# Performance work log

Measured on AMD Instinct MI355X. Metric: run time of the kernel, lower is better.

## Reference

```python
import jax, jax.numpy as jnp
import numpy as np

B, H, DH = 1, 16, 128
HID, MLP = 2048, 8192
LT, LI = 256, 2048
L = LT + LI


def _layernorm(x, eps=1e-6):
    mu = jnp.mean(x, axis=-1, keepdims=True)
    var = jnp.mean((x - mu) ** 2, axis=-1, keepdims=True)
    return (x - mu) * jax.lax.rsqrt(var + eps)


def _rmsnorm(x, scale, eps=1e-6):
    rr = jax.lax.rsqrt(jnp.mean(x * x, axis=-1, keepdims=True) + eps)
    return x * rr * scale


def _apply_rope(x, pe):
    # x: (B,H,L,D) -> (B,H,L,D/2,1,2); pe: (B,1,L,D/2,2,2)
    xs = x.reshape(*x.shape[:-1], -1, 1, 2)
    out = pe[..., 0] * xs[..., 0] + pe[..., 1] * xs[..., 1]  # (B,H,L,D/2,2)
    return out.reshape(x.shape)


def _qkv_split(x, w, b):
    Bv, Lv, _ = x.shape
    qkv = (x @ w + b).reshape(Bv, Lv, 3, H, DH).transpose(2, 0, 3, 1, 4)  # K B H L D
    return qkv[0], qkv[1], qkv[2]


def setup_inputs() -> dict:
    key = jax.random.key(0)
    ks = jax.random.split(key, 16)
    s = 0.02
    inp = {
        'img': jax.random.normal(ks[0], (B, LI, HID), jnp.float32),
        'txt': jax.random.normal(ks[1], (B, LT, HID), jnp.float32),
        'vec': jax.random.normal(ks[2], (B, HID), jnp.float32),
        'img_mod_w': s * jax.random.normal(ks[3], (HID, 6 * HID), jnp.float32),
        'img_mod_b': jnp.zeros((6 * HID,), jnp.float32),
        'txt_mod_w': s * jax.random.normal(ks[4], (HID, 6 * HID), jnp.float32),
        'txt_mod_b': jnp.zeros((6 * HID,), jnp.float32),
        'img_qkv_w': s * jax.random.normal(ks[5], (HID, 3 * HID), jnp.float32),
        'img_qkv_b': jnp.zeros((3 * HID,), jnp.float32),
        'img_q_scale': jnp.ones((DH,), jnp.float32),
        'img_k_scale': jnp.ones((DH,), jnp.float32),
        'txt_qkv_w': s * jax.random.normal(ks[6], (HID, 3 * HID), jnp.float32),
        'txt_qkv_b': jnp.zeros((3 * HID,), jnp.float32),
        'txt_q_scale': jnp.ones((DH,), jnp.float32),
        'txt_k_scale': jnp.ones((DH,), jnp.float32),
        'img_proj_w': s * jax.random.normal(ks[7], (HID, HID), jnp.float32),
        'img_proj_b': jnp.zeros((HID,), jnp.float32),
        'txt_proj_w': s * jax.random.normal(ks[8], (HID, HID), jnp.float32),
        'txt_proj_b': jnp.zeros((HID,), jnp.float32),
        'img_mlp_w1': s * jax.random.normal(ks[9], (HID, MLP), jnp.float32),
        'img_mlp_b1': jnp.zeros((MLP,), jnp.float32),
        'img_mlp_w2': s * jax.random.normal(ks[10], (MLP, HID), jnp.float32),
        'img_mlp_b2': jnp.zeros((HID,), jnp.float32),
        'txt_mlp_w1': s * jax.random.normal(ks[11], (HID, MLP), jnp.float32),
        'txt_mlp_b1': jnp.zeros((MLP,), jnp.float32),
        'txt_mlp_w2': s * jax.random.normal(ks[12], (MLP, HID), jnp.float32),
        'txt_mlp_b2': jnp.zeros((HID,), jnp.float32),
    }
    # Real RoPE rotation matrices [[cos,-sin],[sin,cos]]: (1,1,L,DH/2,2,2)
    pos = jnp.arange(L, dtype=jnp.float32)
    freqs = 1.0 / (10000.0 ** (jnp.arange(DH // 2, dtype=jnp.float32) / (DH // 2)))
    ang = pos[:, None] * freqs[None, :]
    c, sn = jnp.cos(ang), jnp.sin(ang)
    pe = jnp.stack([jnp.stack([c, -sn], -1), jnp.stack([sn, c], -1)], -2)  # (L,DH/2,2,2)
    inp['pe'] = pe[None, None]
    return inp


def reference(img, txt, vec, pe,
              img_mod_w, img_mod_b, txt_mod_w, txt_mod_b,
              img_qkv_w, img_qkv_b, img_q_scale, img_k_scale,
              txt_qkv_w, txt_qkv_b, txt_q_scale, txt_k_scale,
              img_proj_w, img_proj_b, txt_proj_w, txt_proj_b,
              img_mlp_w1, img_mlp_b1, img_mlp_w2, img_mlp_b2,
              txt_mlp_w1, txt_mlp_b1, txt_mlp_w2, txt_mlp_b2):
    # AdaLN modulation: SiLU(vec) @ W -> 6 chunks of (B,1,HID)
    im = jnp.split(jax.nn.silu(vec) @ img_mod_w + img_mod_b, 6, axis=-1)
    i_sh1, i_sc1, i_g1, i_sh2, i_sc2, i_g2 = [m[:, None, :] for m in im]
    tm = jnp.split(jax.nn.silu(vec) @ txt_mod_w + txt_mod_b, 6, axis=-1)
    t_sh1, t_sc1, t_g1, t_sh2, t_sc2, t_g2 = [m[:, None, :] for m in tm]

    img_mod = (1 + i_sc1) * _layernorm(img) + i_sh1
    iq, ik, iv = _qkv_split(img_mod, img_qkv_w, img_qkv_b)
    iq = _rmsnorm(iq, img_q_scale)
    ik = _rmsnorm(ik, img_k_scale)

    txt_mod = (1 + t_sc1) * _layernorm(txt) + t_sh1
    tq, tk, tv = _qkv_split(txt_mod, txt_qkv_w, txt_qkv_b)
    tq = _rmsnorm(tq, txt_q_scale)
    tk = _rmsnorm(tk, txt_k_scale)

    # concat text then image along sequence (B,H,L,D)
    q = jnp.concatenate([tq, iq], axis=2)
    k = jnp.concatenate([tk, ik], axis=2)
    v = jnp.concatenate([tv, iv], axis=2)
    q = _apply_rope(q, pe)
    k = _apply_rope(k, pe)

    scores = jnp.einsum('bhqd,bhkd->bhqk', q, k) / np.float32(np.sqrt(DH))
    a = jax.nn.softmax(scores, axis=-1)
    o = jnp.einsum('bhqk,bhkd->bhqd', a, v)
    attn = o.transpose(0, 2, 1, 3).reshape(o.shape[0], -1, H * DH)  # (B,L,HID)

    txt_a, img_a = attn[:, :LT], attn[:, LT:]

    img = img + i_g1 * (img_a @ img_proj_w + img_proj_b)
    h = (1 + i_sc2) * _layernorm(img) + i_sh2
    h = jax.nn.gelu(h @ img_mlp_w1 + img_mlp_b1, approximate=True)
    img = img + i_g2 * (h @ img_mlp_w2 + img_mlp_b2)

    txt = txt + t_g1 * (txt_a @ txt_proj_w + txt_proj_b)
    h = (1 + t_sc2) * _layernorm(txt) + t_sh2
    h = jax.nn.gelu(h @ txt_mlp_w1 + txt_mlp_b1, approximate=True)
    txt = txt + t_g2 * (h @ txt_mlp_w2 + txt_mlp_b2)

    return img, txt
```

## Files before the change

### kernel.cpp

```cpp
#include <hip/hip_runtime.h>

using u16 = unsigned short;
typedef __bf16 bf16x8 __attribute__((ext_vector_type(8)));
typedef float f32x4 __attribute__((ext_vector_type(4)));

__device__ inline u16 f2bf(float f){
  unsigned u = __float_as_uint(f);
  u += 0x7fff + ((u >> 16) & 1);
  return (u16)(u >> 16);
}
__device__ inline float bf2f(u16 u){ return __uint_as_float((unsigned)u << 16); }

__device__ inline float wredsum(float v){
  #pragma unroll
  for (int o = 32; o; o >>= 1) v += __shfl_xor(v, o, 64);
  return v;
}
__device__ inline float wredmax(float v){
  #pragma unroll
  for (int o = 32; o; o >>= 1) v = fmaxf(v, __shfl_xor(v, o, 64));
  return v;
}

__device__ inline void gld16(const u16* g, u16* lds){
  __builtin_amdgcn_global_load_lds(
      (const __attribute__((address_space(1))) unsigned int*)g,
      (__attribute__((address_space(3))) unsigned int*)lds, 16, 0, 0);
}

__global__ void mod_matvec_k(const float* __restrict__ vec,
    const float* __restrict__ wi, const float* __restrict__ bi,
    const float* __restrict__ wt, const float* __restrict__ bt,
    float* __restrict__ oi, float* __restrict__ ot)
{
  __shared__ float sv[2048];
  __shared__ float red[4][64];
  int tid = threadIdx.x;
  for (int i = tid; i < 2048; i += 256){ float v = vec[i]; sv[i] = v / (1.0f + __expf(-v)); }
  __syncthreads();
  int j0 = blockIdx.x * 64;
  bool ist = j0 >= 12288;
  const float* w = ist ? wt : wi;
  const float* b = ist ? bt : bi;
  float* o = ist ? ot : oi;
  int col = (ist ? j0 - 12288 : j0) + (tid & 63);
  int kq = tid >> 6;
  float acc = 0.f;
  const float* wp = w + col;
  for (int k = kq * 512; k < kq * 512 + 512; ++k) acc += sv[k] * wp[(long long)k * 12288];
  red[kq][tid & 63] = acc;
  __syncthreads();
  if (kq == 0){
    o[col] = red[0][tid] + red[1][tid] + red[2][tid] + red[3][tid] + b[col];
  }
}

__global__ void tcast_k(const float* __restrict__ in, u16* __restrict__ out, int K, int N)
{
  __shared__ float tile[32][33];
  int n0 = blockIdx.x * 32, k0 = blockIdx.y * 32;
  int tid = threadIdx.x;
  int r = tid >> 3, c4 = (tid & 7) * 4;
  float4 v = *(const float4*)&in[(long long)(k0 + r) * N + n0 + c4];
  tile[r][c4 + 0] = v.x; tile[r][c4 + 1] = v.y; tile[r][c4 + 2] = v.z; tile[r][c4 + 3] = v.w;
  __syncthreads();
  int n = tid >> 3, kq = (tid & 7) * 4;
  ushort4 o;
  o.x = f2bf(tile[kq + 0][n]);
  o.y = f2bf(tile[kq + 1][n]);
  o.z = f2bf(tile[kq + 2][n]);
  o.w = f2bf(tile[kq + 3][n]);
  *(ushort4*)&out[(long long)(n0 + n) * K + k0 + kq] = o;
}

__global__ void ln_mod_k(const float* __restrict__ x,
    const float* __restrict__ sh, const float* __restrict__ sc,
    u16* __restrict__ out)
{
  int row = blockIdx.x, tid = threadIdx.x;
  const float* xr = x + (long long)row * 2048;
  float v[8]; float s = 0.f, s2 = 0.f;
  #pragma unroll
  for (int j = 0; j < 8; ++j){ v[j] = xr[tid + j * 256]; s += v[j]; s2 += v[j] * v[j]; }
  s = wredsum(s); s2 = wredsum(s2);
  __shared__ float red[4][2];
  int wave = tid >> 6, lane = tid & 63;
  if (lane == 0){ red[wave][0] = s; red[wave][1] = s2; }
  __syncthreads();
  float S1 = red[0][0] + red[1][0] + red[2][0] + red[3][0];
  float S2 = red[0][1] + red[1][1] + red[2][1] + red[3][1];
  float mu = S1 * (1.0f / 2048.0f);
  float var = S2 * (1.0f / 2048.0f) - mu * mu;
  float rs = rsqrtf(var + 1e-6f);
  u16* orow = out + (long long)row * 2048;
  #pragma unroll
  for (int j = 0; j < 8; ++j){
    int c = tid + j * 256;
    orow[c] = f2bf((1.0f + sc[c]) * (v[j] - mu) * rs + sh[c]);
  }
}

__global__ void qkv_post_k(const float* __restrict__ qkv, int pos0,
    const float* __restrict__ qs, const float* __restrict__ ks,
    const float* __restrict__ pe,
    u16* __restrict__ Q, u16* __restrict__ Ko, u16* __restrict__ Vt)
{
  __shared__ u16 vs[128][72];
  int h = blockIdx.y;
  int t0 = blockIdx.x * 64;
  int tid = threadIdx.x, wave = tid >> 6, lane = tid & 63;
  for (int it = 0; it < 16; ++it){
    int tl = it * 4 + wave;
    int t = t0 + tl;
    const float* rp = qkv + (long long)t * 6144 + h * 128;
    float q0 = rp[lane],        q1 = rp[lane + 64];
    float k0 = rp[2048 + lane], k1 = rp[2048 + lane + 64];
    float v0 = rp[4096 + lane], v1 = rp[4096 + lane + 64];
    float qss = wredsum(q0 * q0 + q1 * q1);
    float kss = wredsum(k0 * k0 + k1 * k1);
    float rq = rsqrtf(qss * (1.0f / 128.0f) + 1e-6f) * 0.08838834764831845f;
    float rk = rsqrtf(kss * (1.0f / 128.0f) + 1e-6f);
    float qn0 = q0 * rq * qs[lane], qn1 = q1 * rq * qs[lane + 64];
    float kn0 = k0 * rk * ks[lane], kn1 = k1 * rk * ks[lane + 64];
    int pos = pos0 + t;
    const float* peb = pe + (long long)pos * 256;
    bool odd = lane & 1;
    float4 p0 = *(const float4*)&peb[(lane >> 1) * 4];
    float4 p1 = *(const float4*)&peb[128 + (lane >> 1) * 4];
    float c00 = odd ? p0.z : p0.x, c01 = odd ? p0.w : p0.y;
    float c10 = odd ? p1.z : p1.x, c11 = odd ? p1.w : p1.y;
    float qp0 = __shfl_xor(qn0, 1, 64), qp1 = __shfl_xor(qn1, 1, 64);
    float kp0 = __shfl_xor(kn0, 1, 64), kp1 = __shfl_xor(kn1, 1, 64);
    float qe0 = odd ? qp0 : qn0, qo0 = odd ? qn0 : qp0;
    float qe1 = odd ? qp1 : qn1, qo1 = odd ? qn1 : qp1;
    float ke0 = odd ? kp0 : kn0, ko0 = odd ? kn0 : kp0;
    float ke1 = odd ? kp1 : kn1, ko1 = odd ? kn1 : kp1;
    u16* Qr = Q  + ((long long)h * 2304 + pos) * 128;
    u16* Kr = Ko + ((long long)h * 2304 + pos) * 128;
    Qr[lane]      = f2bf(c00 * qe0 + c01 * qo0);
    Qr[lane + 64] = f2bf(c10 * qe1 + c11 * qo1);
    Kr[lane]      = f2bf(c00 * ke0 + c01 * ko0);
    Kr[lane + 64] = f2bf(c10 * ke1 + c11 * ko1);
    vs[lane][tl]      = f2bf(v0);
    vs[lane + 64][tl] = f2bf(v1);
  }
  __syncthreads();
  int dd = tid >> 1, co = (tid & 1) * 32;
  u16* vr = Vt + ((long long)h * 128 + dd) * 2304 + pos0 + t0 + co;
  #pragma unroll
  for (int u = 0; u < 8; ++u)
    *(ushort4*)(vr + u * 4) = *(const ushort4*)&vs[dd][co + u * 4];
}

__global__ void softmax16_k(u16* __restrict__ S)
{
  long long base = (long long)blockIdx.y * 2304 * 2304 + (long long)blockIdx.x * 2304;
  u16* row = S + base;
  int tid = threadIdx.x;
  float v[9]; float m = -3.0e38f;
  #pragma unroll
  for (int j = 0; j < 9; ++j){ v[j] = bf2f(row[tid + j * 256]); m = fmaxf(m, v[j]); }
  m = wredmax(m);
  __shared__ float red[4];
  int wave = tid >> 6, lane = tid & 63;
  if (lane == 0) red[wave] = m;
  __syncthreads();
  m = fmaxf(fmaxf(red[0], red[1]), fmaxf(red[2], red[3]));
  float s = 0.f;
  #pragma unroll
  for (int j = 0; j < 9; ++j){ v[j] = __expf(v[j] - m); s += v[j]; }
  s = wredsum(s);
  __syncthreads();
  if (lane == 0) red[wave] = s;
  __syncthreads();
  s = red[0] + red[1] + red[2] + red[3];
  float r = 1.0f / s;
  #pragma unroll
  for (int j = 0; j < 9; ++j) row[tid + j * 256] = f2bf(v[j] * r);
}

template<int MODE>
__global__ __launch_bounds__(512)
void gemm8_k(const u16* __restrict__ Ai, const u16* __restrict__ At, int lda,
             const u16* __restrict__ Bi, const u16* __restrict__ Bt, int ldb,
             const float* __restrict__ bias_i, const float* __restrict__ bias_t,
             const float* __restrict__ res_i,  const float* __restrict__ res_t,
             const float* __restrict__ gate_i, const float* __restrict__ gate_t,
             void* __restrict__ Ci, void* __restrict__ Ct, int ldc, int K)
{
  constexpr int BK = 64;
  constexpr int MR = 4, NR = 2;
  constexpr int AI = 2, BI = 2;

  __shared__ u16 As[2][128 * BK];
  __shared__ u16 Bs[2][128 * BK];

  const int tid  = threadIdx.x;
  const int lane = tid & 63;
  const int wave = tid >> 6;
  const int wm = wave >> 2;
  const int wn = wave & 3;

  const int bx = blockIdx.x;
  const int by = blockIdx.y;
  const bool ist = bx >= 16;
  const int rb = ist ? bx - 16 : bx;
  const u16* Ab = (ist ? At : Ai) + (long long)rb * 128 * lda;
  const u16* Bb = (ist ? Bt : Bi) + (long long)by * 128 * ldb;
  const float* bias = ist ? bias_t : bias_i;
  const float* res  = ist ? res_t  : res_i;
  const float* gate = ist ? gate_t : gate_i;
  void* C = ist ? Ct : Ci;

  const int srow = wave * 8 + (lane >> 3);
  const int sgo  = ((lane & 7) ^ ((lane >> 3) & 7)) * 8;
  const u16* agp[AI]; const u16* bgp[BI];
  int alo[AI], blo[BI];
  #pragma unroll
  for (int i = 0; i < AI; ++i){
    agp[i] = Ab + (long long)(i * 64 + srow) * lda + sgo;
    alo[i] = (i * 64 + wave * 8) * BK;
  }
  #pragma unroll
  for (int i = 0; i < BI; ++i){
    bgp[i] = Bb + (long long)(i * 64 + srow) * ldb + sgo;
    blo[i] = (i * 64 + wave * 8) * BK;
  }

  const int arow0 = wm * 64;
  const int frow  = lane & 15;
  const int fx    = lane & 7;
  const int j0    = lane >> 4;

  f32x4 acc[MR][NR] = {};

  #pragma unroll
  for (int i = 0; i < AI; ++i) gld16(agp[i], &As[0][alo[i]]);
  #pragma unroll
  for (int i = 0; i < BI; ++i) gld16(bgp[i], &Bs[0][blo[i]]);
  __builtin_amdgcn_sched_barrier(0);

  const int nt = K / BK;
  for (int t = 0; t < nt; ++t){
    if (t + 1 < nt){
      int k0 = (t + 1) * BK;
      int nb = (t + 1) & 1;
      #pragma unroll
      for (int i = 0; i < AI; ++i) gld16(agp[i] + k0, &As[nb][alo[i]]);
      #pragma unroll
      for (int i = 0; i < BI; ++i) gld16(bgp[i] + k0, &Bs[nb][blo[i]]);
      __builtin_amdgcn_sched_barrier(0);
      asm volatile("s_waitcnt vmcnt(4)" ::: "memory");
    } else {
      asm volatile("s_waitcnt vmcnt(0)" ::: "memory");
    }
    __builtin_amdgcn_sched_barrier(0);
    __builtin_amdgcn_s_barrier();
    __builtin_amdgcn_sched_barrier(0);

    const u16* as = As[t & 1];
    const u16* bs = Bs[t & 1];
    #pragma unroll
    for (int s = 0; s < 2; ++s){
      const int oct = (s * 4 + j0) ^ fx;
      bf16x8 bfr[NR];
      #pragma unroll
      for (int nn = 0; nn < NR; ++nn)
        bfr[nn] = *(const bf16x8*)&bs[(wn * 32 + nn * 16 + frow) * BK + oct * 8];
      __builtin_amdgcn_s_setprio(1);
      #pragma unroll
      for (int m = 0; m < MR; ++m){
        bf16x8 af = *(const bf16x8*)&as[(arow0 + m * 16 + frow) * BK + oct * 8];
        #pragma unroll
        for (int nn = 0; nn < NR; ++nn)
          acc[m][nn] = __builtin_amdgcn_mfma_f32_16x16x32_bf16(af, bfr[nn], acc[m][nn], 0, 0, 0);
      }
      __builtin_amdgcn_s_setprio(0);
    }
    __builtin_amdgcn_sched_barrier(0);
    __builtin_amdgcn_s_barrier();
    __builtin_amdgcn_sched_barrier(0);
  }

  const int lr = (lane >> 4) * 4;
  const int lc = lane & 15;
  const long long rowb = (long long)rb * 128 + arow0;
  const long long colb = (long long)by * 128 + wn * 32;
  #pragma unroll
  for (int mi = 0; mi < MR; ++mi){
    #pragma unroll
    for (int ni = 0; ni < NR; ++ni){
      long long col = colb + ni * 16 + lc;
      float bv = bias ? bias[col] : 0.0f;
      #pragma unroll
      for (int j = 0; j < 4; ++j){
        long long row = rowb + mi * 16 + lr + j;
        float v = acc[mi][ni][j] + bv;
        long long ci = row * (long long)ldc + col;
        if constexpr (MODE == 0) ((float*)C)[ci] = v;
        else if constexpr (MODE == 2) ((float*)C)[ci] = res[ci] + gate[col] * v;
        else {
          float z2 = 1.5957691216057308f * (v + 0.044715f * v * v * v);
          ((u16*)C)[ci] = f2bf(v / (1.0f + __expf(-z2)));
        }
      }
    }
  }
}

template<int BM, int BN, int MODE>
__global__ __launch_bounds__(256)
void gemm_k(const u16* __restrict__ A, int lda, long long abstr,
            const u16* __restrict__ B, int ldb, long long bbstr,
            void* __restrict__ C, int ldc, long long cbstr,
            int K)
{
  constexpr int BK  = 32;
  constexpr int WGM = BM / 64;
  constexpr int WGN = 4 / WGM;
  constexpr int WTN = BN / WGN;
  constexpr int NFR = WTN / 16;
  constexpr int CA  = BM / 64;
  constexpr int CB  = BN / 64;

  __shared__ u16 As[2][BM * BK];
  __shared__ u16 Bs[2][BN * BK];
  const int tid  = threadIdx.x;
  const int lane = tid & 63;
  const int wave = tid >> 6;
  const int wr = (wave / WGN) * 64;
  const int wc = (wave % WGN) * WTN;

  const u16* Ab = A + (long long)blockIdx.z * abstr + (long long)blockIdx.x * BM * lda;
  const u16* Bb = B + (long long)blockIdx.z * bbstr + (long long)blockIdx.y * BN * ldb;

  const int srow = lane >> 2;
  const int scol = (lane & 3) * 8;
  const u16* agp[CA]; int aro[CA];
  const u16* bgp[CB]; int bro[CB];
  #pragma unroll
  for (int c = 0; c < CA; ++c){
    int r0 = (c * 4 + wave) * 16;
    agp[c] = Ab + (long long)(r0 + srow) * lda + scol;
    aro[c] = r0 * BK;
  }
  #pragma unroll
  for (int c = 0; c < CB; ++c){
    int r0 = (c * 4 + wave) * 16;
    bgp[c] = Bb + (long long)(r0 + srow) * ldb + scol;
    bro[c] = r0 * BK;
  }

  #pragma unroll
  for (int c = 0; c < CA; ++c) gld16(agp[c], &As[0][aro[c]]);
  #pragma unroll
  for (int c = 0; c < CB; ++c) gld16(bgp[c], &Bs[0][bro[c]]);
  __syncthreads();

  f32x4 acc[4][NFR] = {};
  const int nt = K / BK;
  int cur = 0;
  for (int t = 0; t < nt; ++t){
    int nxt = cur ^ 1;
    if (t + 1 < nt){
      int ko = (t + 1) * BK;
      #pragma unroll
      for (int c = 0; c < CA; ++c) gld16(agp[c] + ko, &As[nxt][aro[c]]);
      #pragma unroll
      for (int c = 0; c < CB; ++c) gld16(bgp[c] + ko, &Bs[nxt][bro[c]]);
    }
    bf16x8 af[4], bfr[NFR];
    #pragma unroll
    for (int i = 0; i < 4; ++i)
      af[i] = *(const bf16x8*)&As[cur][(wr + i * 16 + (lane & 15)) * BK + (lane >> 4) * 8];
    #pragma unroll
    for (int i = 0; i < NFR; ++i)
      bfr[i] = *(const bf16x8*)&Bs[cur][(wc + i * 16 + (lane & 15)) * BK + (lane >> 4) * 8];
    #pragma unroll
    for (int mi = 0; mi < 4; ++mi)
      #pragma unroll
      for (int ni = 0; ni < NFR; ++ni)
        acc[mi][ni] = __builtin_amdgcn_mfma_f32_16x16x32_bf16(af[mi], bfr[ni], acc[mi][ni], 0, 0, 0);
    __syncthreads();
    cur = nxt;
  }

  const int lr = (lane >> 4) * 4;
  const int lc = lane & 15;
  const long long rowb = (long long)blockIdx.x * BM + wr;
  const long long colb = (long long)blockIdx.y * BN + wc;
  const long long cb = (long long)blockIdx.z * cbstr;
  #pragma unroll
  for (int mi = 0; mi < 4; ++mi){
    #pragma unroll
    for (int ni = 0; ni < NFR; ++ni){
      long long col = colb + ni * 16 + lc;
      #pragma unroll
      for (int j = 0; j < 4; ++j){
        long long row = rowb + mi * 16 + lr + j;
        float v = acc[mi][ni][j];
        long long ci = cb + row * ldc + col;
        if constexpr (MODE == 0) ((float*)C)[ci] = v;
        else ((u16*)C)[ci] = f2bf(v);
      }
    }
  }
}

extern "C" void kernel_launch(void* const* d_in, const int* in_sizes, int n_in,
                              void* d_out, int out_size, void* d_ws, size_t ws_size,
                              hipStream_t stream)
{
  const float* img        = (const float*)d_in[0];
  const float* txt        = (const float*)d_in[1];
  const float* vec        = (const float*)d_in[2];
  const float* img_mod_w  = (const float*)d_in[3];
  const float* img_mod_b  = (const float*)d_in[4];
  const float* txt_mod_w  = (const float*)d_in[5];
  const float* txt_mod_b  = (const float*)d_in[6];
  const float* img_qkv_w  = (const float*)d_in[7];
  const float* img_qkv_b  = (const float*)d_in[8];
  const float* img_q_s    = (const float*)d_in[9];
  const float* img_k_s    = (const float*)d_in[10];
  const float* txt_qkv_w  = (const float*)d_in[11];
  const float* txt_qkv_b  = (const float*)d_in[12];
  const float* txt_q_s    = (const float*)d_in[13];
  const float* txt_k_s    = (const float*)d_in[14];
  const float* img_proj_w = (const float*)d_in[15];
  const float* img_proj_b = (const float*)d_in[16];
  const float* txt_proj_w = (const float*)d_in[17];
  const float* txt_proj_b = (const float*)d_in[18];
  const float* img_mlp_w1 = (const float*)d_in[19];
  const float* img_mlp_b1 = (const float*)d_in[20];
  const float* img_mlp_w2 = (const float*)d_in[21];
  const float* img_mlp_b2 = (const float*)d_in[22];
  const float* txt_mlp_w1 = (const float*)d_in[23];
  const float* txt_mlp_b1 = (const float*)d_in[24];
  const float* txt_mlp_w2 = (const float*)d_in[25];
  const float* txt_mlp_b2 = (const float*)d_in[26];
  const float* pe         = (const float*)d_in[27];

  char* ws = (char*)d_ws;
  size_t off = 0;
  auto alloc = [&](size_t b){ void* p = ws + off; off = (off + b + 255) & ~(size_t)255; return p; };

  u16* wq_i = (u16*)alloc(6144ll * 2048 * 2);
  u16* wq_t = (u16*)alloc(6144ll * 2048 * 2);
  u16* wp_i = (u16*)alloc(2048ll * 2048 * 2);
  u16* wp_t = (u16*)alloc(2048ll * 2048 * 2);
  u16* w1_i = (u16*)alloc(8192ll * 2048 * 2);
  u16* w1_t = (u16*)alloc(8192ll * 2048 * 2);
  u16* w2_i = (u16*)alloc(2048ll * 8192 * 2);
  u16* w2_t = (u16*)alloc(2048ll * 8192 * 2);
  float* mod_i = (float*)alloc(12288 * 4);
  float* mod_t = (float*)alloc(12288 * 4);
  u16* Qb   = (u16*)alloc(16ll * 2304 * 128 * 2);
  u16* Kb   = (u16*)alloc(16ll * 2304 * 128 * 2);
  u16* Vt   = (u16*)alloc(16ll * 2304 * 128 * 2);
  u16* attn = (u16*)alloc(2304ll * 2048 * 2);
  char* big = (char*)alloc(4ll * 2304 * 2304 * 4);

  size_t s16_bytes = 16ll * 2304 * 2304 * 2;
  size_t off_before_s16 = off;
  u16* S16 = (u16*)alloc(s16_bytes);
  const bool merged_attn = (off <= ws_size);
  if (!merged_attn) off = off_before_s16;

  u16*   xin_i = (u16*)big;
  u16*   xin_t = (u16*)(big + 8388608);
  float* qkv_i = (float*)(big + 9437184);
  float* qkv_t = (float*)(big + 59768832);
  u16*   S4   = (u16*)big;
  float* y1_i  = (float*)big;
  float* y1_t  = (float*)(big + 16777216);
  u16*   ln2_i = (u16*)(big + 18874368);
  u16*   ln2_t = (u16*)(big + 27262976);
  u16*   h_i   = (u16*)(big + 28311552);
  u16*   h_t   = (u16*)(big + 61865984);

  mod_matvec_k<<<384, 256, 0, stream>>>(vec, img_mod_w, img_mod_b, txt_mod_w, txt_mod_b, mod_i, mod_t);

  tcast_k<<<dim3(192, 64), 256, 0, stream>>>(img_qkv_w, wq_i, 2048, 6144);
  tcast_k<<<dim3(192, 64), 256, 0, stream>>>(txt_qkv_w, wq_t, 2048, 6144);
  tcast_k<<<dim3(64, 64),  256, 0, stream>>>(img_proj_w, wp_i, 2048, 2048);
  tcast_k<<<dim3(64, 64),  256, 0, stream>>>(txt_proj_w, wp_t, 2048, 2048);
  tcast_k<<<dim3(256, 64), 256, 0, stream>>>(img_mlp_w1, w1_i, 2048, 8192);
  tcast_k<<<dim3(256, 64), 256, 0, stream>>>(txt_mlp_w1, w1_t, 2048, 8192);
  tcast_k<<<dim3(64, 256), 256, 0, stream>>>(img_mlp_w2, w2_i, 8192, 2048);
  tcast_k<<<dim3(64, 256), 256, 0, stream>>>(txt_mlp_w2, w2_t, 8192, 2048);

  ln_mod_k<<<2048, 256, 0, stream>>>(img, mod_i, mod_i + 2048, xin_i);
  ln_mod_k<<<256,  256, 0, stream>>>(txt, mod_t, mod_t + 2048, xin_t);

  gemm8_k<0><<<dim3(18, 48), 512, 0, stream>>>(xin_i, xin_t, 2048, wq_i, wq_t, 2048,
      img_qkv_b, txt_qkv_b, nullptr, nullptr, nullptr, nullptr, qkv_i, qkv_t, 6144, 2048);

  qkv_post_k<<<dim3(32, 16), 256, 0, stream>>>(qkv_i, 256, img_q_s, img_k_s, pe, Qb, Kb, Vt);
  qkv_post_k<<<dim3(4, 16),  256, 0, stream>>>(qkv_t, 0,   txt_q_s, txt_k_s, pe, Qb, Kb, Vt);

  if (merged_attn){
    gemm_k<128,128,1><<<dim3(18, 18, 16), 256, 0, stream>>>(Qb, 128, 2304ll * 128, Kb, 128, 2304ll * 128,
        S16, 2304, 2304ll * 2304, 128);
    softmax16_k<<<dim3(2304, 16), 256, 0, stream>>>(S16);
    gemm_k<128,64,1><<<dim3(18, 2, 16), 256, 0, stream>>>(S16, 2304, 2304ll * 2304, Vt, 2304, 128ll * 2304,
        attn, 2048, 128, 2304);
  } else {
    for (int g = 0; g < 4; ++g){
      const u16* Qg = Qb + (long long)g * 4 * 2304 * 128;
      const u16* Kg = Kb + (long long)g * 4 * 2304 * 128;
      const u16* Vg = Vt + (long long)g * 4 * 128 * 2304;
      gemm_k<128,128,1><<<dim3(18, 18, 4), 256, 0, stream>>>(Qg, 128, 2304ll * 128, Kg, 128, 2304ll * 128,
          S4, 2304, 2304ll * 2304, 128);
      softmax16_k<<<dim3(2304, 4), 256, 0, stream>>>(S4);
      gemm_k<128,64,1><<<dim3(18, 2, 4), 256, 0, stream>>>(S4, 2304, 2304ll * 2304, Vg, 2304, 128ll * 2304,
          attn + g * 4 * 128, 2048, 128, 2304);
    }
  }

  gemm8_k<2><<<dim3(18, 16), 512, 0, stream>>>(attn + 256 * 2048, attn, 2048, wp_i, wp_t, 2048,
      img_proj_b, txt_proj_b, img, txt, mod_i + 4096, mod_t + 4096, y1_i, y1_t, 2048, 2048);

  ln_mod_k<<<2048, 256, 0, stream>>>(y1_i, mod_i + 6144, mod_i + 8192, ln2_i);
  ln_mod_k<<<256,  256, 0, stream>>>(y1_t, mod_t + 6144, mod_t + 8192, ln2_t);

  gemm8_k<3><<<dim3(18, 64), 512, 0, stream>>>(ln2_i, ln2_t, 2048, w1_i, w1_t, 2048,
      img_mlp_b1, txt_mlp_b1, nullptr, nullptr, nullptr, nullptr, h_i, h_t, 8192, 2048);

  float* out_img = (float*)d_out;
  float* out_txt = out_img + 2048ll * 2048;
  gemm8_k<2><<<dim3(18, 16), 512, 0, stream>>>(h_i, h_t, 8192, w2_i, w2_t, 8192,
      img_mlp_b2, txt_mlp_b2, y1_i, y1_t, mod_i + 10240, mod_t + 10240, out_img, out_txt, 2048, 8192);
}
```

Measured before the change: 906.3 us.

## Batch weight transpose-casts into one launch and remap GEMM workgroups across XCDs

Merges the eight separate weight transpose-and-cast launches into a single grid kernel that picks its matrix through a per-matrix block-offset table, which removes per-launch overhead and tail gaps between launches. It also remaps workgroup ids in gemm8_k so that consecutive tiles land on the same XCD (ids are strided by 8), with the aim of better L2 reuse of shared A and B tiles. The remap assumes the tile count is divisible by 8 and adds a short index search per block in the cast kernel.

```diff
diff --git a/kernel.cpp b/kernel.cpp
--- a/kernel.cpp
+++ b/kernel.cpp
@@ -55,10 +55,27 @@
   }
 }
 
-__global__ void tcast_k(const float* __restrict__ in, u16* __restrict__ out, int K, int N)
+struct TcArgs {
+  const float* in[8];
+  u16* out[8];
+  int K[8];
+  int N[8];
+  int base[9];
+};
+
+__global__ void tcast8_k(TcArgs a)
 {
   __shared__ float tile[32][33];
-  int n0 = blockIdx.x * 32, k0 = blockIdx.y * 32;
+  int bid = blockIdx.x;
+  int w = 0;
+  #pragma unroll
+  for (int i = 0; i < 8; ++i) if (bid >= a.base[i + 1]) w = i + 1;
+  const float* in = a.in[w];
+  u16* out = a.out[w];
+  int K = a.K[w], N = a.N[w];
+  int local = bid - a.base[w];
+  int tx = N >> 5;
+  int n0 = (local % tx) * 32, k0 = (local / tx) * 32;
   int tid = threadIdx.x;
   int r = tid >> 3, c4 = (tid & 7) * 4;
   float4 v = *(const float4*)&in[(long long)(k0 + r) * N + n0 + c4];
@@ -201,8 +218,13 @@
   const int wm = wave >> 2;
   const int wn = wave & 3;
 
-  const int bx = blockIdx.x;
-  const int by = blockIdx.y;
+  const int gx = gridDim.x;
+  const int nwg = gx * gridDim.y;
+  const int n = blockIdx.x + gx * blockIdx.y;
+  const int s_id = (n & 7) * (nwg >> 3) + (n >> 3);
+  const int bx = s_id % gx;
+  const int by = s_id / gx;
+
   const bool ist = bx >= 16;
   const int rb = ist ? bx - 16 : bx;
   const u16* Ab = (ist ? At : Ai) + (long long)rb * 128 * lda;
@@ -480,14 +502,22 @@
 
   mod_matvec_k<<<384, 256, 0, stream>>>(vec, img_mod_w, img_mod_b, txt_mod_w, txt_mod_b, mod_i, mod_t);
 
-  tcast_k<<<dim3(192, 64), 256, 0, stream>>>(img_qkv_w, wq_i, 2048, 6144);
-  tcast_k<<<dim3(192, 64), 256, 0, stream>>>(txt_qkv_w, wq_t, 2048, 6144);
-  tcast_k<<<dim3(64, 64),  256, 0, stream>>>(img_proj_w, wp_i, 2048, 2048);
-  tcast_k<<<dim3(64, 64),  256, 0, stream>>>(txt_proj_w, wp_t, 2048, 2048);
-  tcast_k<<<dim3(256, 64), 256, 0, stream>>>(img_mlp_w1, w1_i, 2048, 8192);
-  tcast_k<<<dim3(256, 64), 256, 0, stream>>>(txt_mlp_w1, w1_t, 2048, 8192);
-  tcast_k<<<dim3(64, 256), 256, 0, stream>>>(img_mlp_w2, w2_i, 8192, 2048);
-  tcast_k<<<dim3(64, 256), 256, 0, stream>>>(txt_mlp_w2, w2_t, 8192, 2048);
+  {
+    TcArgs a;
+    const float* ins[8] = {img_qkv_w, txt_qkv_w, img_proj_w, txt_proj_w,
+                           img_mlp_w1, txt_mlp_w1, img_mlp_w2, txt_mlp_w2};
+    u16* outs[8] = {wq_i, wq_t, wp_i, wp_t, w1_i, w1_t, w2_i, w2_t};
+    int Ks[8] = {2048, 2048, 2048, 2048, 2048, 2048, 8192, 8192};
+    int Ns[8] = {6144, 6144, 2048, 2048, 8192, 8192, 2048, 2048};
+    int b = 0;
+    for (int i = 0; i < 8; ++i){
+      a.in[i] = ins[i]; a.out[i] = outs[i]; a.K[i] = Ks[i]; a.N[i] = Ns[i];
+      a.base[i] = b;
+      b += (Ks[i] >> 5) * (Ns[i] >> 5);
+    }
+    a.base[8] = b;
+    tcast8_k<<<b, 256, 0, stream>>>(a);
+  }
 
   ln_mod_k<<<2048, 256, 0, stream>>>(img, mod_i, mod_i + 2048, xin_i);
   ln_mod_k<<<256,  256, 0, stream>>>(txt, mod_t, mod_t + 2048, xin_t);
```

Result: faster. 883.7 us (-2.5%).
